# Performance work log

Measured on AMD Instinct MI355X. Metric: run time of the kernel, lower is better.

The kernel has to match this reference:

```python
import jax, jax.numpy as jnp
import numpy as np

B, S, D = 8, 1025, 768
H, KV, HD = 12, 4, 64
GH, GW = 32, 32
EPS = 1e-6


def setup_inputs() -> dict:
    key = jax.random.key(0)
    ks = jax.random.split(key, 6)
    sc = 0.02
    hidden_states = jax.random.normal(ks[0], (B, S, D), jnp.float32)
    attention_mask = jnp.ones((B, S), dtype=bool)
    image_pos_ids = jnp.broadcast_to(jnp.arange(S, dtype=jnp.int32), (B, S))
    return dict(
        hidden_states=hidden_states,
        attention_mask=attention_mask,
        image_pos_ids=image_pos_ids,
        grid_h=GH,
        grid_w=GW,
        Wq=jax.random.normal(ks[1], (D, H * HD), jnp.float32) * sc,
        Wk=jax.random.normal(ks[2], (D, KV * HD), jnp.float32) * sc,
        Wv=jax.random.normal(ks[3], (D, KV * HD), jnp.float32) * sc,
        Wo=jax.random.normal(ks[4], (H * HD, D), jnp.float32) * sc,
        q_norm_w=jnp.ones((HD,), jnp.float32),
        k_norm_w=jnp.ones((HD,), jnp.float32),
    )


def _rmsnorm(x, w, eps=EPS):
    return x * jax.lax.rsqrt(jnp.mean(x * x, axis=-1, keepdims=True) + eps) * w


def _rotate(x, cos, sin):
    # x: [B, h, P, HD]; cos/sin: [B, P, HD//2]. Pairs are adjacent (view_as_complex).
    hd = x.shape[-1]
    xr = x.reshape(*x.shape[:-1], hd // 2, 2)
    x0, x1 = xr[..., 0], xr[..., 1]
    c, s = cos[:, None], sin[:, None]  # broadcast over heads
    o0 = x0 * c - x1 * s
    o1 = x0 * s + x1 * c
    return jnp.stack([o0, o1], axis=-1).reshape(x.shape)


def reference(hidden_states, attention_mask, image_pos_ids, grid_h, grid_w,
              Wq, Wk, Wv, Wo, q_norm_w, k_norm_w):
    b, s, d = hidden_states.shape
    hd = q_norm_w.shape[0]
    h = Wq.shape[1] // hd
    kv = Wk.shape[1] // hd
    n_rep = h // kv
    scale = hd ** -0.5

    q = _rmsnorm((hidden_states @ Wq).reshape(b, s, h, hd), q_norm_w).transpose(0, 2, 1, 3)
    k = _rmsnorm((hidden_states @ Wk).reshape(b, s, kv, hd), k_norm_w).transpose(0, 2, 1, 3)
    v = (hidden_states @ Wv).reshape(b, s, kv, hd).transpose(0, 2, 1, 3)

    # 2D RoPE on patch tokens only (CLS token at position 0 excluded)
    ids = image_pos_ids[:, 1:]
    hi = (ids // grid_w) % grid_h
    wi = ids % grid_w
    half, quarter = hd // 2, hd // 4
    inv_freq = 1.0 / (10000.0 ** (jnp.arange(quarter, dtype=jnp.float32) * 2.0 / half))
    ang = jnp.concatenate([hi[..., None] * inv_freq, wi[..., None] * inv_freq], axis=-1)  # [B,P,HD/2]
    cos, sin = jnp.cos(ang), jnp.sin(ang)
    q = jnp.concatenate([q[:, :, :1], _rotate(q[:, :, 1:], cos, sin)], axis=2)
    k = jnp.concatenate([k[:, :, :1], _rotate(k[:, :, 1:], cos, sin)], axis=2)

    # GQA: repeat_interleave kv heads to match query heads
    kr = jnp.repeat(k, n_rep, axis=1)
    vr = jnp.repeat(v, n_rep, axis=1)

    scores = jnp.einsum('bhqd,bhkd->bhqk', q, kr) * scale
    add = jnp.where(attention_mask, 0.0, jnp.finfo(jnp.float32).min)[:, None, None, :]
    scores = scores + add
    attn = jax.nn.softmax(scores.astype(jnp.float32), axis=-1).astype(q.dtype)
    out = jnp.einsum('bhqk,bhkd->bqhd', attn, vr).reshape(b, s, h * hd)
    return (out @ Wo, attn)
```

## Files before the change

kernel.cpp:

```cpp
#include <hip/hip_runtime.h>

#define B_ 8
#define S_ 1025
#define D_ 768
#define H_ 12
#define KV_ 4
#define HD_ 64
#define NREP 3
#define SCALE_ 0.125f
#define EPS_ 1e-6f
#define SKP 1088
#define SCS 1092
#define PST 1096
#define QBLK 16
#define NQT 65

typedef __attribute__((ext_vector_type(8))) short bf16x8;
typedef __attribute__((ext_vector_type(4))) float f32x4;

__device__ __forceinline__ unsigned short f2bf(float f) {
  unsigned int u = __builtin_bit_cast(unsigned int, f);
  return (unsigned short)((u + 0x7FFFu + ((u >> 16) & 1u)) >> 16);
}
__device__ __forceinline__ unsigned int pk2(float a, float b) {
  return (unsigned int)f2bf(a) | ((unsigned int)f2bf(b) << 16);
}

__global__ __launch_bounds__(256) void cast_x_kernel(const float* __restrict__ x,
                                                     unsigned short* __restrict__ xb, int n4) {
  int i = blockIdx.x * 256 + threadIdx.x;
  if (i >= n4) return;
  f32x4 v = *(const f32x4*)(x + (size_t)i * 4);
  uint2 o;
  o.x = pk2(v[0], v[1]);
  o.y = pk2(v[2], v[3]);
  *(uint2*)(xb + (size_t)i * 4) = o;
}

__global__ __launch_bounds__(256) void cast_wqkv_kernel(const float* __restrict__ Wq,
    const float* __restrict__ Wk, const float* __restrict__ Wv,
    unsigned short* __restrict__ WT) {
  int idx = blockIdx.x * 256 + threadIdx.x;
  int n = idx / D_, k = idx % D_;
  float v;
  if (n < 768)       v = Wq[(size_t)k * 768 + n];
  else if (n < 1024) v = Wk[(size_t)k * 256 + (n - 768)];
  else               v = Wv[(size_t)k * 256 + (n - 1024)];
  WT[idx] = f2bf(v);
}

__global__ __launch_bounds__(256) void cast_wo_kernel(const float* __restrict__ Wo,
                                                      unsigned short* __restrict__ WT) {
  int idx = blockIdx.x * 256 + threadIdx.x;
  int n = idx / D_, k = idx % D_;
  WT[idx] = f2bf(Wo[(size_t)k * D_ + n]);
}

#define BM 128
#define BN 128
#define BK 32
#define LSTR 40
__global__ __launch_bounds__(256) void gemm_bt(const unsigned short* __restrict__ A,
    const unsigned short* __restrict__ BT, float* __restrict__ C, int M, int N, int K) {
  __shared__ unsigned short As[BM * LSTR];
  __shared__ unsigned short Bs[BN * LSTR];
  const int nMt = (M + BM - 1) / BM;
  const int tm = blockIdx.x % nMt;
  const int tn = blockIdx.x / nMt;
  const int row0 = tm * BM, col0 = tn * BN;
  const int tid = threadIdx.x;
  const int l = tid & 63, w = tid >> 6;
  const int wr = (w >> 1) * 64, wc = (w & 1) * 64;
  const int lr = l & 15, lk = (l >> 4) * 8;
  f32x4 acc[4][4] = {};
  for (int kt = 0; kt < K; kt += BK) {
    __syncthreads();
#pragma unroll
    for (int i = 0; i < 2; ++i) {
      int c = tid + i * 256;
      int r = c >> 2;
      int ce = (c & 3) * 8;
      int gr = row0 + r; gr = gr < M ? gr : M - 1;
      bf16x8 va = *(const bf16x8*)(A + (size_t)gr * K + kt + ce);
      *(bf16x8*)&As[r * LSTR + ce] = va;
      bf16x8 vb = *(const bf16x8*)(BT + (size_t)(col0 + r) * K + kt + ce);
      *(bf16x8*)&Bs[r * LSTR + ce] = vb;
    }
    __syncthreads();
    bf16x8 af[4], bfr[4];
#pragma unroll
    for (int m = 0; m < 4; ++m)
      af[m] = *(const bf16x8*)&As[(wr + m * 16 + lr) * LSTR + lk];
#pragma unroll
    for (int n = 0; n < 4; ++n)
      bfr[n] = *(const bf16x8*)&Bs[(wc + n * 16 + lr) * LSTR + lk];
#pragma unroll
    for (int m = 0; m < 4; ++m)
#pragma unroll
      for (int n = 0; n < 4; ++n)
        acc[m][n] = __builtin_amdgcn_mfma_f32_16x16x32_bf16(af[m], bfr[n], acc[m][n], 0, 0, 0);
  }
  const int orow = (l >> 4) * 4;
#pragma unroll
  for (int m = 0; m < 4; ++m)
#pragma unroll
    for (int n = 0; n < 4; ++n)
#pragma unroll
      for (int r = 0; r < 4; ++r) {
        int row = row0 + wr + m * 16 + orow + r;
        int col = col0 + wc + n * 16 + lr;
        if (row < M) C[(size_t)row * N + col] = acc[m][n][r];
      }
}

__global__ __launch_bounds__(256) void qkv_epilogue(const float* __restrict__ QKV,
    const int* __restrict__ pos_ids, const int* __restrict__ ghp, const int* __restrict__ gwp,
    const float* __restrict__ qw, const float* __restrict__ kw,
    unsigned short* __restrict__ Qb, unsigned short* __restrict__ Kb,
    unsigned short* __restrict__ Vt) {
  int tok = blockIdx.x * 4 + (threadIdx.x >> 6);
  int l = threadIdx.x & 63;
  if (tok >= B_ * S_) return;
  int b = tok / S_, s = tok % S_;
  const float* rowp = QKV + (size_t)tok * 1280;
  bool rot = (s > 0);
  float cs = 1.f, sn = 0.f;
  if (rot) {
    int gh = ghp[0], gw = gwp[0];
    int pos = pos_ids[tok];
    int hi = (pos / gw) % gh;
    int wi = pos % gw;
    int pi = l >> 1;
    int j = pi < 16 ? pi : pi - 16;
    float invf = exp2f(-(float)j * (13.287712379549449f / 16.f));
    float ang = (pi < 16 ? (float)hi : (float)wi) * invf;
    cs = cosf(ang); sn = sinf(ang);
  }
#pragma unroll
  for (int h = 0; h < H_; ++h) {
    float x = rowp[h * 64 + l];
    float ss = x * x;
    for (int off = 32; off; off >>= 1) ss += __shfl_xor(ss, off);
    float xn = x * rsqrtf(ss * (1.f / 64.f) + EPS_) * qw[l];
    float o = xn;
    if (rot) {
      float p = __shfl_xor(xn, 1);
      o = (l & 1) ? (p * sn + xn * cs) : (xn * cs - p * sn);
    }
    o *= SCALE_;
    Qb[((size_t)(b * H_ + h) * S_ + s) * 64 + l] = f2bf(o);
  }
#pragma unroll
  for (int h = 0; h < KV_; ++h) {
    float x = rowp[768 + h * 64 + l];
    float ss = x * x;
    for (int off = 32; off; off >>= 1) ss += __shfl_xor(ss, off);
    float xn = x * rsqrtf(ss * (1.f / 64.f) + EPS_) * kw[l];
    float o = xn;
    if (rot) {
      float p = __shfl_xor(xn, 1);
      o = (l & 1) ? (p * sn + xn * cs) : (xn * cs - p * sn);
    }
    Kb[((size_t)(b * KV_ + h) * S_ + s) * 64 + l] = f2bf(o);
    float v = rowp[1024 + h * 64 + l];
    Vt[((size_t)(b * KV_ + h) * 64 + l) * SKP + s] = f2bf(v);
  }
}

__global__ __launch_bounds__(512, 4) void attn_kernel(const unsigned short* __restrict__ Qb,
    const unsigned short* __restrict__ Kb, const unsigned short* __restrict__ Vt,
    unsigned short* __restrict__ ctx, float* __restrict__ attn_out) {
  extern __shared__ float Sc[];
  __shared__ float partial[4][64][4];
  int bid = blockIdx.x;
  int swz = (bid & 7) * 780 + (bid >> 3);
  int qt = swz % NQT;
  int h = (swz / NQT) % H_;
  int b = swz / (NQT * H_);
  int kvh = h / NREP;
  int q0 = qt * QBLK;
  int tid = threadIdx.x;
  int l = tid & 63, w = tid >> 6;
  int lr = l & 15, lk = (l >> 4) * 8;

  const unsigned short* Qbase = Qb + (size_t)(b * H_ + h) * S_ * 64;
  const unsigned short* Kbase = Kb + (size_t)(b * KV_ + kvh) * S_ * 64;
  const unsigned short* Vbase = Vt + (size_t)(b * KV_ + kvh) * 64 * SKP;

  int qrow = q0 + lr; if (qrow >= S_) qrow = S_ - 1;
  bf16x8 qf0 = *(const bf16x8*)(Qbase + (size_t)qrow * 64 + lk);
  bf16x8 qf1 = *(const bf16x8*)(Qbase + (size_t)qrow * 64 + 32 + lk);

  {
    const int kcol = w * 16 + lr;
    const int nT = (w < 4) ? 9 : 8;
    const unsigned short* kp = Kbase + (size_t)kcol * 64;
    bf16x8 kf0 = *(const bf16x8*)(kp + lk);
    bf16x8 kf1 = *(const bf16x8*)(kp + 32 + lk);
    for (int t = 0; t < nT; ++t) {
      bf16x8 nf0 = kf0, nf1 = kf1;
      if (t + 1 < nT) {
        int kr = (t + 1) * 128 + kcol; if (kr >= S_) kr = S_ - 1;
        const unsigned short* np = Kbase + (size_t)kr * 64;
        nf0 = *(const bf16x8*)(np + lk);
        nf1 = *(const bf16x8*)(np + 32 + lk);
      }
      f32x4 acc = {};
      acc = __builtin_amdgcn_mfma_f32_16x16x32_bf16(qf0, kf0, acc, 0, 0, 0);
      acc = __builtin_amdgcn_mfma_f32_16x16x32_bf16(qf1, kf1, acc, 0, 0, 0);
      int col = t * 128 + kcol;
      int rowb = (l >> 4) * 4;
#pragma unroll
      for (int r = 0; r < 4; ++r) Sc[(size_t)(rowb + r) * SCS + col] = acc[r];
      kf0 = nf0; kf1 = nf1;
    }
  }
  __syncthreads();

  float vals[2][17];
#pragma unroll
  for (int rr = 0; rr < 2; ++rr) {
    int rowi = w + rr * 8;
    const float* srow = Sc + (size_t)rowi * SCS;
    float mx = -1e30f;
#pragma unroll
    for (int i = 0; i < 17; ++i) {
      int key = l + i * 64;
      float v = (key < S_) ? srow[key] : -1e30f;
      vals[rr][i] = v;
      mx = fmaxf(mx, v);
    }
    for (int off = 32; off; off >>= 1) mx = fmaxf(mx, __shfl_xor(mx, off));
    float sum = 0.f;
#pragma unroll
    for (int i = 0; i < 17; ++i) {
      float e = __expf(vals[rr][i] - mx);
      vals[rr][i] = e; sum += e;
    }
    for (int off = 32; off; off >>= 1) sum += __shfl_xor(sum, off);
    float inv = 1.f / sum;
#pragma unroll
    for (int i = 0; i < 17; ++i) {
      int key = l + i * 64;
      vals[rr][i] = (key < S_) ? vals[rr][i] * inv : 0.f;
    }
  }
  __syncthreads();

  {
    unsigned short* P = (unsigned short*)Sc;
#pragma unroll
    for (int rr = 0; rr < 2; ++rr) {
      int rowi = w + rr * 8;
      unsigned short* prow = P + (size_t)rowi * PST;
#pragma unroll
      for (int i = 0; i < 17; ++i) prow[l + i * 64] = f2bf(vals[rr][i]);
    }
  }
  __syncthreads();

  f32x4 accv = {};
  {
    const int d0 = (w & 3) * 16;
    const int kh = (w >> 2) * 544;
    const unsigned short* U = (const unsigned short*)Sc;
    const int prow = lr * PST;
    const unsigned short* vb = Vbase + (size_t)(d0 + lr) * SKP + kh;
#pragma unroll 4
    for (int kc = 0; kc < 17; ++kc) {
      bf16x8 pa = *(const bf16x8*)&U[prow + kh + kc * 32 + lk];
      bf16x8 vf = *(const bf16x8*)(vb + kc * 32 + lk);
      accv = __builtin_amdgcn_mfma_f32_16x16x32_bf16(pa, vf, accv, 0, 0, 0);
    }
  }
  if (w >= 4) *(f32x4*)partial[w - 4][l] = accv;
  __syncthreads();
  if (w < 4) {
    accv += *(const f32x4*)partial[w][l];
    int rowb = (l >> 4) * 4;
    int d0 = (w & 3) * 16;
#pragma unroll
    for (int r = 0; r < 4; ++r) {
      int q = q0 + rowb + r;
      if (q < S_)
        ctx[(size_t)(b * S_ + q) * 768 + h * 64 + d0 + lr] = f2bf(accv[r]);
    }
  }

#pragma unroll
  for (int rr = 0; rr < 2; ++rr) {
    int q = q0 + w + rr * 8;
    if (q < S_) {
      float* gout = attn_out + ((size_t)(b * H_ + h) * S_ + q) * S_;
#pragma unroll
      for (int i = 0; i < 16; ++i)
        __builtin_nontemporal_store(vals[rr][i], gout + l + i * 64);
      if (l == 0) __builtin_nontemporal_store(vals[rr][16], gout + 1024);
    }
  }
}

extern "C" void kernel_launch(void* const* d_in, const int* in_sizes, int n_in,
                              void* d_out, int out_size, void* d_ws, size_t ws_size,
                              hipStream_t stream) {
  const float* hidden = (const float*)d_in[0];
  const int* pos_ids = (const int*)d_in[2];
  const int* ghp = (const int*)d_in[3];
  const int* gwp = (const int*)d_in[4];
  const float* Wq = (const float*)d_in[5];
  const float* Wk = (const float*)d_in[6];
  const float* Wv = (const float*)d_in[7];
  const float* Wo = (const float*)d_in[8];
  const float* qnw = (const float*)d_in[9];
  const float* knw = (const float*)d_in[10];

  char* ws = (char*)d_ws;
  unsigned short* Xb    = (unsigned short*)ws;
  unsigned short* WqkvT = (unsigned short*)(ws + 12595200);
  unsigned short* WoT   = (unsigned short*)(ws + 14561280);
  float*          QKV   = (float*)(ws + 15740928);
  unsigned short* ctx   = (unsigned short*)(ws + 15740928);
  unsigned short* Qb    = (unsigned short*)(ws + 57724928);
  unsigned short* Kb    = (unsigned short*)(ws + 70320128);
  unsigned short* Vt    = (unsigned short*)(ws + 74518528);

  float* out0 = (float*)d_out;
  float* attn_out = out0 + (size_t)B_ * S_ * D_;

  cast_x_kernel<<<6150, 256, 0, stream>>>(hidden, Xb, 1574400);
  cast_wqkv_kernel<<<3840, 256, 0, stream>>>(Wq, Wk, Wv, WqkvT);
  cast_wo_kernel<<<2304, 256, 0, stream>>>(Wo, WoT);

  gemm_bt<<<65 * 10, 256, 0, stream>>>(Xb, WqkvT, QKV, B_ * S_, 1280, D_);

  hipMemsetAsync(Vt, 0, 4456448, stream);
  qkv_epilogue<<<2050, 256, 0, stream>>>(QKV, pos_ids, ghp, gwp, qnw, knw, Qb, Kb, Vt);

  hipFuncSetAttribute((const void*)attn_kernel,
                      hipFuncAttributeMaxDynamicSharedMemorySize, QBLK * SCS * 4);
  attn_kernel<<<B_ * H_ * NQT, 512, QBLK * SCS * 4, stream>>>(Qb, Kb, Vt, ctx, attn_out);

  gemm_bt<<<65 * 6, 256, 0, stream>>>(ctx, WoT, out0, B_ * S_, D_, D_);
}
```

Baseline: 354.8 us.

## Store attention scores as fp16 in LDS and defer softmax normalization

The attention kernel now keeps the score tile in LDS as fp16 instead of fp32, which halves the dynamic shared memory, and raises the launch-bounds occupancy hint from 4 to 8. Softmax keeps the unnormalized exponentials in fewer registers. The 1/sum factor is applied later, to the PV output and when the probabilities are written back from the bf16 LDS copy. Storing scores in fp16 and writing attn from bf16 probabilities lowers precision of both scores and the returned attention matrix, and relies on fp16 range for scores.

```diff
diff --git a/kernel.cpp b/kernel.cpp
--- a/kernel.cpp
+++ b/kernel.cpp
@@ -1,4 +1,5 @@
 #include <hip/hip_runtime.h>
+#include <hip/hip_fp16.h>
 
 #define B_ 8
 #define S_ 1025
@@ -10,13 +11,15 @@
 #define SCALE_ 0.125f
 #define EPS_ 1e-6f
 #define SKP 1088
-#define SCS 1092
+#define HSS 1092
 #define PST 1096
 #define QBLK 16
 #define NQT 65
+#define DYNLDS 35072
 
 typedef __attribute__((ext_vector_type(8))) short bf16x8;
 typedef __attribute__((ext_vector_type(4))) float f32x4;
+typedef __attribute__((ext_vector_type(2))) float f32x2;
 
 __device__ __forceinline__ unsigned short f2bf(float f) {
   unsigned int u = __builtin_bit_cast(unsigned int, f);
@@ -24,6 +27,9 @@
 }
 __device__ __forceinline__ unsigned int pk2(float a, float b) {
   return (unsigned int)f2bf(a) | ((unsigned int)f2bf(b) << 16);
+}
+__device__ __forceinline__ float bf2f(unsigned int u) {
+  return __builtin_bit_cast(float, u << 16);
 }
 
 __global__ __launch_bounds__(256) void cast_x_kernel(const float* __restrict__ x,
@@ -167,11 +173,12 @@
   }
 }
 
-__global__ __launch_bounds__(512, 4) void attn_kernel(const unsigned short* __restrict__ Qb,
+__global__ __launch_bounds__(512, 8) void attn_kernel(const unsigned short* __restrict__ Qb,
     const unsigned short* __restrict__ Kb, const unsigned short* __restrict__ Vt,
     unsigned short* __restrict__ ctx, float* __restrict__ attn_out) {
-  extern __shared__ float Sc[];
+  extern __shared__ unsigned short Ush[];
   __shared__ float partial[4][64][4];
+  __shared__ float invsh[16];
   int bid = blockIdx.x;
   int swz = (bid & 7) * 780 + (bid >> 3);
   int qt = swz % NQT;
@@ -211,51 +218,60 @@
       int col = t * 128 + kcol;
       int rowb = (l >> 4) * 4;
 #pragma unroll
-      for (int r = 0; r < 4; ++r) Sc[(size_t)(rowb + r) * SCS + col] = acc[r];
+      for (int r = 0; r < 4; ++r)
+        Ush[(size_t)(rowb + r) * HSS + col] =
+            __builtin_bit_cast(unsigned short, __float2half(acc[r]));
       kf0 = nf0; kf1 = nf1;
     }
   }
   __syncthreads();
 
-  float vals[2][17];
+  float invr[2];
+  float ta[2], tasum;
+  f32x2 ef[2][8];
 #pragma unroll
   for (int rr = 0; rr < 2; ++rr) {
     int rowi = w + rr * 8;
-    const float* srow = Sc + (size_t)rowi * SCS;
-    float mx = -1e30f;
-#pragma unroll
-    for (int i = 0; i < 17; ++i) {
-      int key = l + i * 64;
-      float v = (key < S_) ? srow[key] : -1e30f;
-      vals[rr][i] = v;
-      mx = fmaxf(mx, v);
-    }
+    const unsigned short* Hrow = Ush + (size_t)rowi * HSS;
+    f32x2 f[8];
+#pragma unroll
+    for (int i = 0; i < 8; ++i) {
+      __half2 hv = *(const __half2*)&Hrow[i * 128 + 2 * l];
+      float2 fv = __half22float2(hv);
+      f[i][0] = fv.x; f[i][1] = fv.y;
+    }
+    float tail = __half2float(*(const __half*)&Hrow[1024]);
+    if (l != 0) tail = -1e30f;
+    float mx = tail;
+#pragma unroll
+    for (int i = 0; i < 8; ++i) mx = fmaxf(mx, fmaxf(f[i][0], f[i][1]));
     for (int off = 32; off; off >>= 1) mx = fmaxf(mx, __shfl_xor(mx, off));
     float sum = 0.f;
 #pragma unroll
-    for (int i = 0; i < 17; ++i) {
-      float e = __expf(vals[rr][i] - mx);
-      vals[rr][i] = e; sum += e;
-    }
+    for (int i = 0; i < 8; ++i) {
+      f[i][0] = __expf(f[i][0] - mx); f[i][1] = __expf(f[i][1] - mx);
+      sum += f[i][0] + f[i][1];
+      ef[rr][i] = f[i];
+    }
+    float te = __expf(tail - mx);
+    ta[rr] = te;
+    sum += te;
     for (int off = 32; off; off >>= 1) sum += __shfl_xor(sum, off);
-    float inv = 1.f / sum;
-#pragma unroll
-    for (int i = 0; i < 17; ++i) {
-      int key = l + i * 64;
-      vals[rr][i] = (key < S_) ? vals[rr][i] * inv : 0.f;
-    }
-  }
+    invr[rr] = 1.f / sum;
+  }
+  tasum = ta[0];  (void)tasum;
   __syncthreads();
 
-  {
-    unsigned short* P = (unsigned short*)Sc;
-#pragma unroll
-    for (int rr = 0; rr < 2; ++rr) {
-      int rowi = w + rr * 8;
-      unsigned short* prow = P + (size_t)rowi * PST;
-#pragma unroll
-      for (int i = 0; i < 17; ++i) prow[l + i * 64] = f2bf(vals[rr][i]);
-    }
+#pragma unroll
+  for (int rr = 0; rr < 2; ++rr) {
+    int rowi = w + rr * 8;
+    unsigned short* Prow = Ush + (size_t)rowi * PST;
+#pragma unroll
+    for (int i = 0; i < 8; ++i)
+      *(unsigned int*)&Prow[i * 128 + 2 * l] = pk2(ef[rr][i][0], ef[rr][i][1]);
+    if (l < 32)
+      *(unsigned int*)&Prow[1024 + 2 * l] = (l == 0) ? pk2(ta[rr], 0.f) : 0u;
+    if (l == 0) invsh[rowi] = invr[rr];
   }
   __syncthreads();
 
@@ -263,12 +279,11 @@
   {
     const int d0 = (w & 3) * 16;
     const int kh = (w >> 2) * 544;
-    const unsigned short* U = (const unsigned short*)Sc;
     const int prow = lr * PST;
     const unsigned short* vb = Vbase + (size_t)(d0 + lr) * SKP + kh;
 #pragma unroll 4
     for (int kc = 0; kc < 17; ++kc) {
-      bf16x8 pa = *(const bf16x8*)&U[prow + kh + kc * 32 + lk];
+      bf16x8 pa = *(const bf16x8*)&Ush[prow + kh + kc * 32 + lk];
       bf16x8 vf = *(const bf16x8*)(vb + kc * 32 + lk);
       accv = __builtin_amdgcn_mfma_f32_16x16x32_bf16(pa, vf, accv, 0, 0, 0);
     }
@@ -283,19 +298,30 @@
     for (int r = 0; r < 4; ++r) {
       int q = q0 + rowb + r;
       if (q < S_)
-        ctx[(size_t)(b * S_ + q) * 768 + h * 64 + d0 + lr] = f2bf(accv[r]);
+        ctx[(size_t)(b * S_ + q) * 768 + h * 64 + d0 + lr] = f2bf(accv[r] * invsh[rowb + r]);
     }
   }
 
 #pragma unroll
   for (int rr = 0; rr < 2; ++rr) {
-    int q = q0 + w + rr * 8;
+    int rowi = w + rr * 8;
+    int q = q0 + rowi;
     if (q < S_) {
+      float inv = invr[rr];
+      const unsigned short* Prow = Ush + (size_t)rowi * PST;
       float* gout = attn_out + ((size_t)(b * H_ + h) * S_ + q) * S_;
 #pragma unroll
-      for (int i = 0; i < 16; ++i)
-        __builtin_nontemporal_store(vals[rr][i], gout + l + i * 64);
-      if (l == 0) __builtin_nontemporal_store(vals[rr][16], gout + 1024);
+      for (int i = 0; i < 8; ++i) {
+        unsigned int d = *(const unsigned int*)&Prow[i * 128 + 2 * l];
+        f32x2 o;
+        o[0] = bf2f(d & 0xffffu) * inv;
+        o[1] = bf2f(d >> 16) * inv;
+        __builtin_nontemporal_store(o, (f32x2*)(gout + i * 128 + 2 * l));
+      }
+      if (l == 0) {
+        unsigned int d = *(const unsigned int*)&Prow[1024];
+        __builtin_nontemporal_store(bf2f(d & 0xffffu) * inv, gout + 1024);
+      }
     }
   }
 }
@@ -337,8 +363,8 @@
   qkv_epilogue<<<2050, 256, 0, stream>>>(QKV, pos_ids, ghp, gwp, qnw, knw, Qb, Kb, Vt);
 
   hipFuncSetAttribute((const void*)attn_kernel,
-                      hipFuncAttributeMaxDynamicSharedMemorySize, QBLK * SCS * 4);
-  attn_kernel<<<B_ * H_ * NQT, 512, QBLK * SCS * 4, stream>>>(Qb, Kb, Vt, ctx, attn_out);
+                      hipFuncAttributeMaxDynamicSharedMemorySize, DYNLDS);
+  attn_kernel<<<B_ * H_ * NQT, 512, DYNLDS, stream>>>(Qb, Kb, Vt, ctx, attn_out);
 
   gemm_bt<<<65 * 6, 256, 0, stream>>>(ctx, WoT, out0, B_ * S_, D_, D_);
 }
```

Measured after the change: 340.0 us. -4.2%, faster.
